# Kernel tuning notes

Measured on AMD Instinct MI355X. Metric: run time of the kernel, lower is better.

The kernel has to match this reference:

```python
import jax, jax.numpy as jnp
import numpy as np

EPS = 1e-5
K_NEIGH = 8


def _conv1(x, w, b):
    # x: [B,C,N], w: [O,C], b: [O] -> [B,O,N]  (1x1 Conv1d)
    return jnp.einsum('bcn,oc->bon', x, w) + b[None, :, None]


def _bn(x, g, b):
    # BatchNorm1d in training mode: stats over (B, N)
    m = jnp.mean(x, axis=(0, 2), keepdims=True)
    v = jnp.var(x, axis=(0, 2), keepdims=True)
    return g[None, :, None] * (x - m) * jax.lax.rsqrt(v + EPS) + b[None, :, None]


def _get_local_diffs(x, k):
    # x: [B,N,C] -> [B, 2C, N]
    xyz = x[:, :, :3]
    sq = jnp.sum(xyz * xyz, axis=-1)  # [B,N]
    d2 = sq[:, :, None] + sq[:, None, :] - 2.0 * jnp.einsum('bnc,bmc->bnm', xyz, xyz)
    dists = jnp.sqrt(jnp.maximum(d2, 0.0))  # [B,N,N]
    _, idx = jax.lax.top_k(-dists, k + 1)   # smallest distances
    idx = idx[:, :, 1:]                     # drop self -> [B,N,k]
    neigh = jax.vmap(lambda xi, ii: xi[ii])(x, idx)  # [B,N,k,C]
    diff_mean = jnp.mean(neigh, axis=2) - x          # [B,N,C]
    out = jnp.concatenate([diff_mean, x], axis=2)    # [B,N,2C]
    return jnp.transpose(out, (0, 2, 1))             # [B,2C,N]


def _forward(x, w1, b1, g1, be1, w2, b2, g2, be2, w3, b3, g3, be3,
             qw, qb, kw, kb, vw, vb, fw, fb, aw1, ab1, aw2, ab2, fcw, fcb):
    h = _get_local_diffs(x, K_NEIGH)                 # [B,18,N]
    h = jax.nn.relu(_bn(_conv1(h, w1, b1), g1, be1))  # [B,64,N]
    h = jax.nn.relu(_bn(_conv1(h, w2, b2), g2, be2))  # [B,128,N]
    h = jax.nn.relu(_bn(_conv1(h, w3, b3), g3, be3))  # [B,256,N]
    # global attention
    Q = _conv1(h, qw, qb)  # [B,H,N]
    Kt = _conv1(h, kw, kb)
    V = _conv1(h, vw, vb)
    attn = jax.nn.softmax(jnp.einsum('bhn,bhm->bnm', Q, Kt), axis=-1)  # [B,N,N]
    o = jnp.einsum('bhm,bnm->bhn', V, attn)
    h = _conv1(o, fw, fb) + h
    # attention pooling
    a = jax.nn.relu(_conv1(h, aw1, ab1))
    s = _conv1(a, aw2, ab2)                 # [B,1,N]
    w = jax.nn.softmax(s, axis=-1)
    pooled = jnp.sum(h * w, axis=-1)        # [B,256]
    return jax.nn.relu(pooled @ fcw.T + fcb)  # [B,256]


def setup_inputs() -> dict:
    key = jax.random.key(0)
    ks = jax.random.split(key, 32)
    B, N, C = 4, 4096, 9
    HID = 128

    def p(i, shape, scale=0.05):
        return (jax.random.normal(ks[i], shape, dtype=jnp.float32) * scale)

    inp = {'x': jax.random.normal(ks[0], (B, N, C), dtype=jnp.float32)}
    dims = [(2 * C, 64), (64, 128), (128, 256)]
    for li, (ci, co) in enumerate(dims, start=1):
        inp[f'w{li}'] = p(li, (co, ci))
        inp[f'b{li}'] = p(li + 3, (co,))
        inp[f'g{li}'] = jnp.ones((co,), jnp.float32)
        inp[f'be{li}'] = jnp.zeros((co,), jnp.float32)
    Cf = 256
    inp['qw'] = p(7, (HID, Cf)); inp['qb'] = p(8, (HID,))
    inp['kw'] = p(9, (HID, Cf)); inp['kb'] = p(10, (HID,))
    inp['vw'] = p(11, (HID, Cf)); inp['vb'] = p(12, (HID,))
    inp['fw'] = p(13, (Cf, HID)); inp['fb'] = p(14, (Cf,))
    inp['aw1'] = p(15, (64, Cf)); inp['ab1'] = p(16, (64,))
    inp['aw2'] = p(17, (1, 64)); inp['ab2'] = p(18, (1,))
    inp['fcw'] = p(19, (256, Cf)); inp['fcb'] = p(20, (256,))
    return inp


def reference(x, w1, b1, g1, be1, w2, b2, g2, be2, w3, b3, g3, be3,
              qw, qb, kw, kb, vw, vb, fw, fb, aw1, ab1, aw2, ab2, fcw, fcb):
    return _forward(x, w1, b1, g1, be1, w2, b2, g2, be2, w3, b3, g3, be3,
                    qw, qb, kw, kb, vw, vb, fw, fb, aw1, ab1, aw2, ab2, fcw, fcb)
```

## Files before the change

kernel.cpp:

```cpp
#include <hip/hip_runtime.h>
#include <math.h>

constexpr int B    = 4;
constexpr int NPTS = 4096;
constexpr int NTOT = B * NPTS;
constexpr int CIN  = 9;
constexpr int C0   = 18;
constexpr int KNB  = 8;
constexpr int HID  = 128;
constexpr int QR   = 64;
constexpr int KC   = 64;
constexpr int NSPL = 4;
constexpr float EPSF = 1e-5f;

using f32x4  = __attribute__((ext_vector_type(4))) float;
using bf16x8 = __attribute__((ext_vector_type(8))) short;

__device__ inline unsigned short f2bf(float f) {
    unsigned int x = __float_as_uint(f);
    unsigned int r = (x + 0x7fffu + ((x >> 16) & 1u)) >> 16;
    return (unsigned short)r;
}
__device__ inline float bf2f(unsigned short u) {
    return __uint_as_float(((unsigned int)u) << 16);
}
__device__ inline unsigned int pack2(float a, float b) {
    return (unsigned int)f2bf(a) | ((unsigned int)f2bf(b) << 16);
}

#define GLD_LDS16(g, l) __builtin_amdgcn_global_load_lds( \
    (const __attribute__((address_space(1))) void*)(g),   \
    (__attribute__((address_space(3))) void*)(l), 16, 0, 0)

__global__ __launch_bounds__(256) void prep_kernel(const float* __restrict__ x,
                                                   float4* __restrict__ xyzw,
                                                   const float* __restrict__ w2,
                                                   const float* __restrict__ w3,
                                                   const float* __restrict__ qw,
                                                   const float* __restrict__ kw,
                                                   const float* __restrict__ vw,
                                                   const float* __restrict__ fw,
                                                   const float* __restrict__ aw1,
                                                   unsigned short* __restrict__ dst) {
    const int i = blockIdx.x * 256 + threadIdx.x;
    if (i < NTOT) {
        const float* xp = x + (size_t)i * CIN;
        const float a = xp[0], b = xp[1], c = xp[2];
        xyzw[i] = make_float4(a, b, c, a * a + b * b + c * c);
    }
    const float* src;
    int off;
    if      (i <   8192) { src = w2;  off = 0; }
    else if (i <  40960) { src = w3;  off = 8192; }
    else if (i <  73728) { src = qw;  off = 40960; }
    else if (i < 106496) { src = kw;  off = 73728; }
    else if (i < 139264) { src = vw;  off = 106496; }
    else if (i < 172032) { src = fw;  off = 139264; }
    else                 { src = aw1; off = 172032; }
    dst[i] = f2bf(src[i - off]);
}

__global__ __launch_bounds__(256) void knn3_kernel(const float* __restrict__ x,
                                                   const float4* __restrict__ xyzw,
                                                   float* __restrict__ h0) {
    __shared__ __align__(16) char lds[16384];
    const int tid = threadIdx.x;
    const int w = tid >> 6, l = tid & 63;
    const int b  = blockIdx.x >> 9;
    const int p0 = (blockIdx.x & 511) << 3;
    const int c  = l & 31;
    const int p  = w * 2 + (l >> 5);
    const int n  = p0 + p;
    const float4* xb4 = xyzw + (size_t)b * NPTS;

    const float4 q4 = xb4[n];
    const float qx = q4.x, qy = q4.y, qz = q4.z, sqn = q4.w;

    float bd[KNB];
    int   bi[KNB];
#pragma unroll
    for (int i = 0; i < KNB; ++i) { bd[i] = 3.0e38f; bi[i] = 0; }

    auto stage = [&](int buf, int t) {
#pragma unroll
        for (int i = 0; i < 2; ++i) {
            const int idx = i * 256 + w * 64 + l;
            const int m   = idx ^ ((idx >> 4) & 7);
            GLD_LDS16(xb4 + (size_t)t * 512 + m, lds + buf * 8192 + i * 4096 + w * 1024);
        }
    };

    stage(0, 0);
    for (int t = 0; t < 8; ++t) {
        const int cur = t & 1;
        __syncthreads();
        if (t < 7) stage(cur ^ 1, t + 1);

        float thr = bd[KNB - 1];
        thr = fminf(thr, __shfl_xor(thr, 1));
        thr = fminf(thr, __shfl_xor(thr, 2));
        thr = fminf(thr, __shfl_xor(thr, 4));
        thr = fminf(thr, __shfl_xor(thr, 8));
        thr = fminf(thr, __shfl_xor(thr, 16));

        const char* buf = lds + cur * 8192 + c * 256;
        const int mbase = t * 512 + c * 16;
        const int cswz  = (c & 7) << 4;
#pragma unroll 4
        for (int j = 0; j < 16; ++j) {
            const float4 f4 = *(const float4*)(buf + ((j << 4) ^ cswz));
            const float tt = fmaf(qx, f4.x, fmaf(qy, f4.y, qz * f4.z));
            const float d2 = fmaf(-2.0f, tt, sqn + f4.w);
            const int m = mbase + j;
            const float gate = fminf(thr, bd[KNB - 1]);
            if (d2 < gate && m != n) {
                bd[KNB - 1] = d2; bi[KNB - 1] = m;
#pragma unroll
                for (int s = KNB - 1; s > 0; --s) {
                    if (bd[s] < bd[s - 1]) {
                        float td = bd[s]; bd[s] = bd[s - 1]; bd[s - 1] = td;
                        int   ti = bi[s]; bi[s] = bi[s - 1]; bi[s - 1] = ti;
                    }
                }
            }
        }
    }

    int res[KNB];
    const int lh = l & 31;
#pragma unroll
    for (int r = 0; r < KNB; ++r) {
        float hd = bd[0]; int hb = bi[0]; int hl = lh;
#pragma unroll
        for (int mask = 16; mask > 0; mask >>= 1) {
            const float od = __shfl_xor(hd, mask);
            const int   ob = __shfl_xor(hb, mask);
            const int   ol = __shfl_xor(hl, mask);
            if (od < hd || (od == hd && ol < hl)) { hd = od; hb = ob; hl = ol; }
        }
        res[r] = hb;
        if (lh == hl) {
#pragma unroll
            for (int s = 0; s < KNB - 1; ++s) { bd[s] = bd[s + 1]; bi[s] = bi[s + 1]; }
            bd[KNB - 1] = 3.0e38f;
        }
    }

    const int c8 = c & 7;
    int nb = res[0];
#pragma unroll
    for (int k = 1; k < KNB; ++k) nb = (c8 == k) ? res[k] : nb;
    const float* xb = x + (size_t)b * NPTS * CIN;
    float nv[CIN];
    const float* nbp = xb + (size_t)nb * CIN;
#pragma unroll
    for (int ch = 0; ch < CIN; ++ch) nv[ch] = nbp[ch];
#pragma unroll
    for (int d = 1; d < 8; d <<= 1) {
#pragma unroll
        for (int ch = 0; ch < CIN; ++ch) nv[ch] += __shfl_xor(nv[ch], d);
    }
    const int ch = min(c, 8);
    float nvc = nv[0];
#pragma unroll
    for (int k = 1; k < CIN; ++k) nvc = (ch == k) ? nv[k] : nvc;
    if (c < 9) {
        const float xv = xb[(size_t)n * CIN + ch];
        h0[((size_t)b * C0 + ch) * NPTS + n]       = nvc * 0.125f - xv;
        h0[((size_t)b * C0 + CIN + ch) * NPTS + n] = xv;
    }
}

__global__ __launch_bounds__(256) void conv1_kernel(const float* __restrict__ X,
                                                    const float* __restrict__ W,
                                                    const float* __restrict__ bias,
                                                    float* __restrict__ Y,
                                                    float* __restrict__ parts) {
    __shared__ float Ws[16 * C0];
    const int b  = blockIdx.z;
    const int o_base = blockIdx.y * 16;
    const int l  = threadIdx.x & 63;
    const int n  = blockIdx.x * 64 + l;
    const int og = threadIdx.x >> 6;
    for (int i = threadIdx.x; i < 16 * C0; i += 256)
        Ws[i] = W[(size_t)o_base * C0 + i];
    __syncthreads();
    float acc[4] = {0.f, 0.f, 0.f, 0.f};
    const float* Xp = X + (size_t)b * C0 * NPTS + n;
    for (int c = 0; c < C0; ++c) {
        const float xv = Xp[(size_t)c * NPTS];
#pragma unroll
        for (int i = 0; i < 4; ++i)
            acc[i] = fmaf(Ws[(og * 4 + i) * C0 + c], xv, acc[i]);
    }
    f32x4 v;
#pragma unroll
    for (int i = 0; i < 4; ++i) v[i] = acc[i] + bias[o_base + og * 4 + i];
    *(f32x4*)(Y + ((size_t)b * NPTS + n) * 64 + o_base + og * 4) = v;
    float s1[4], s2[4];
#pragma unroll
    for (int i = 0; i < 4; ++i) { s1[i] = v[i]; s2[i] = v[i] * v[i]; }
#pragma unroll
    for (int d = 1; d < 64; d <<= 1) {
#pragma unroll
        for (int i = 0; i < 4; ++i) {
            s1[i] += __shfl_xor(s1[i], d);
            s2[i] += __shfl_xor(s2[i], d);
        }
    }
    if (l == 0) {
        const int rg = blockIdx.z * 64 + blockIdx.x;
#pragma unroll
        for (int i = 0; i < 4; ++i) {
            const int ch = o_base + og * 4 + i;
            parts[ch * 256 + rg]            = s1[i];
            parts[64 * 256 + ch * 256 + rg] = s2[i];
        }
    }
}

__global__ __launch_bounds__(64) void finstats_kernel(const float* __restrict__ parts,
                                                      float* __restrict__ mstats, int O) {
    const int ch = blockIdx.x, l = threadIdx.x;
    const f32x4 a1 = *(const f32x4*)(parts + (size_t)ch * 256 + l * 4);
    const f32x4 a2 = *(const f32x4*)(parts + (size_t)O * 256 + (size_t)ch * 256 + l * 4);
    float s1 = (a1[0] + a1[1]) + (a1[2] + a1[3]);
    float s2 = (a2[0] + a2[1]) + (a2[2] + a2[3]);
#pragma unroll
    for (int d = 1; d < 64; d <<= 1) {
        s1 += __shfl_xor(s1, d);
        s2 += __shfl_xor(s2, d);
    }
    if (l == 0) {
        const float mean = s1 * (1.0f / NTOT);
        const float var  = s2 * (1.0f / NTOT) - mean * mean;
        mstats[ch]     = mean;
        mstats[O + ch] = rsqrtf(var + EPSF);
    }
}

__global__ __launch_bounds__(256) void bnapply_kernel(const float* __restrict__ Y,
                                                      const float* __restrict__ mstats,
                                                      const float* __restrict__ g,
                                                      const float* __restrict__ be,
                                                      unsigned short* __restrict__ Yb,
                                                      int O) {
    const size_t i4 = (size_t)blockIdx.x * 256 + threadIdx.x;
    const int cbase = (int)((i4 * 4) & (O - 1));
    const f32x4 v = *(const f32x4*)(Y + i4 * 4);
    ushort4 pk;
    unsigned short* pp = (unsigned short*)&pk;
#pragma unroll
    for (int r = 0; r < 4; ++r) {
        const int c = cbase + r;
        const float y = fmaxf(g[c] * mstats[O + c] * (v[r] - mstats[c]) + be[c], 0.f);
        pp[r] = f2bf(y);
    }
    *(ushort4*)(Yb + i4 * 4) = pk;
}

template <int C, int EPI>
__global__ __launch_bounds__(256) void gemm_kernel(const unsigned short* __restrict__ A,
                                                   const unsigned short* __restrict__ Wb,
                                                   const float* __restrict__ bias,
                                                   const unsigned short* __restrict__ resid,
                                                   void* __restrict__ Yv, int O,
                                                   float* __restrict__ parts) {
    constexpr int RB = 2 * C;
    constexpr int SLOTS = C / 8;
    __shared__ __align__(16) char ldsW[64 * RB];
    const int tid = threadIdx.x;
    const int w = tid >> 6, l = tid & 63;
    const int lg = l >> 4, lq = l & 15;
    const int n0 = blockIdx.x * 64;
    const int o0 = blockIdx.y * 64;

#pragma unroll
    for (int i = 0; i < C / 32; ++i) {
        const int idx = i * 256 + tid;
        const int m  = idx / SLOTS;
        const int sl = (idx % SLOTS) ^ (m & 7);
        GLD_LDS16(Wb + (size_t)(o0 + m) * C + sl * 8, ldsW + (i * 256 + w * 64) * 16);
    }

    const int nr = n0 + w * 16 + lq;
    const unsigned short* Ap = A + (size_t)nr * C + lg * 8;
    f32x4 acc[4];
#pragma unroll
    for (int os = 0; os < 4; ++os) acc[os] = {0.f, 0.f, 0.f, 0.f};
    __syncthreads();

#pragma unroll
    for (int ks = 0; ks < C / 32; ++ks) {
        const bf16x8 af = *(const bf16x8*)(Ap + ks * 32);
#pragma unroll
        for (int os = 0; os < 4; ++os) {
            const int row = os * 16 + lq;
            const bf16x8 wf = *(const bf16x8*)(ldsW + ((row * RB + ks * 64 + lg * 16) ^ ((lq & 7) << 4)));
            acc[os] = __builtin_amdgcn_mfma_f32_16x16x32_bf16(wf, af, acc[os], 0, 0, 0);
        }
    }

    f32x4 vv[4];
#pragma unroll
    for (int os = 0; os < 4; ++os) {
        const int ob = o0 + os * 16 + lg * 4;
        const f32x4 bv = *(const f32x4*)(bias + ob);
#pragma unroll
        for (int r = 0; r < 4; ++r) vv[os][r] = acc[os][r] + bv[r];
        if (EPI == 0) {
            *(f32x4*)((float*)Yv + (size_t)nr * O + ob) = vv[os];
        } else if (EPI == 4) {
            unsigned short* Y = (unsigned short*)Yv;
            const int bb = nr >> 12, n = nr & (NPTS - 1);
#pragma unroll
            for (int r = 0; r < 4; ++r)
                Y[((size_t)bb * HID + ob + r) * NPTS + n] = f2bf(vv[os][r]);
        } else {
            f32x4 v = vv[os];
            if (EPI == 3) {
                const ushort4 rv = *(const ushort4*)(resid + (size_t)nr * O + ob);
                v[0] += bf2f(rv.x); v[1] += bf2f(rv.y); v[2] += bf2f(rv.z); v[3] += bf2f(rv.w);
            }
            if (EPI == 2) {
#pragma unroll
                for (int r = 0; r < 4; ++r) v[r] = fmaxf(v[r], 0.f);
            }
            ushort4 pk;
            pk.x = f2bf(v[0]); pk.y = f2bf(v[1]); pk.z = f2bf(v[2]); pk.w = f2bf(v[3]);
            *(ushort4*)((unsigned short*)Yv + (size_t)nr * O + ob) = pk;
        }
    }

    if (EPI == 0) {
        float* sred = (float*)ldsW;
        float s1[4][4], s2[4][4];
#pragma unroll
        for (int os = 0; os < 4; ++os)
#pragma unroll
            for (int r = 0; r < 4; ++r) {
                float a1 = vv[os][r], a2 = vv[os][r] * vv[os][r];
#pragma unroll
                for (int d = 1; d < 16; d <<= 1) {
                    a1 += __shfl_xor(a1, d);
                    a2 += __shfl_xor(a2, d);
                }
                s1[os][r] = a1; s2[os][r] = a2;
            }
        __syncthreads();
        if (lq == 0) {
#pragma unroll
            for (int os = 0; os < 4; ++os)
#pragma unroll
                for (int r = 0; r < 4; ++r) {
                    const int ch = os * 16 + lg * 4 + r;
                    sred[(w * 64 + ch) * 2 + 0] = s1[os][r];
                    sred[(w * 64 + ch) * 2 + 1] = s2[os][r];
                }
        }
        __syncthreads();
        if (tid < 128) {
            const int ch = tid & 63, st = tid >> 6;
            const float a = sred[ch * 2 + st] + sred[(64 + ch) * 2 + st]
                          + sred[(128 + ch) * 2 + st] + sred[(192 + ch) * 2 + st];
            parts[(size_t)st * O * 256 + (size_t)(o0 + ch) * 256 + blockIdx.x] = a;
        }
    }
}

__device__ __forceinline__ void stage_tile(char* lds, int buf,
                                           const unsigned short* Kb,
                                           const unsigned short* Vb,
                                           int n0, int w, int l) {
    char* dK = lds + buf * 16384;
    char* dV = lds + 32768 + buf * 16384;
#pragma unroll
    for (int j = 0; j < 4; ++j) {
        const int y = w * 4096 + j * 1024 + l * 16;
        const int m = y >> 8;
        const int slot = ((y >> 4) & 15) ^ (m & 7);
        GLD_LDS16(Kb + (size_t)(n0 + m) * HID + slot * 8, dK + w * 4096 + j * 1024);
    }
#pragma unroll
    for (int j = 0; j < 4; ++j) {
        const int y = w * 4096 + j * 1024 + l * 16;
        const int h = y >> 7;
        const int slot = ((y >> 4) & 7) ^ (h & 7);
        GLD_LDS16(Vb + (size_t)h * NPTS + n0 + slot * 8, dV + w * 4096 + j * 1024);
    }
}

__global__ __launch_bounds__(256) void fmha2_kernel(const unsigned short* __restrict__ Qg,
                                                    const unsigned short* __restrict__ Kg,
                                                    const unsigned short* __restrict__ Vg,
                                                    float* __restrict__ A0, float* __restrict__ A1,
                                                    float* __restrict__ A2, float* __restrict__ A3,
                                                    float* __restrict__ Mb, float* __restrict__ Lb) {
    __shared__ __align__(16) char lds[73728];
    const int tid = threadIdx.x;
    const int w = tid >> 6, l = tid & 63;
    const int lg = l >> 4, lq = l & 15;
    const int b  = blockIdx.y;
    const int q0 = blockIdx.x * QR;
    const int split = blockIdx.z;
    const int n0base = split * (NPTS / NSPL);
    float* Ap = (split == 0) ? A0 : (split == 1) ? A1 : (split == 2) ? A2 : A3;
    float* Mp = Mb + split * NTOT;
    float* Lp = Lb + split * NTOT;
    char* ldsP = lds + 65536 + w * 2048;

    bf16x8 qf[4];
    {
        const unsigned short* qp = Qg + ((size_t)b * NPTS + q0 + w * 16 + lq) * HID + lg * 8;
#pragma unroll
        for (int ks = 0; ks < 4; ++ks)
            qf[ks] = *(const bf16x8*)(qp + ks * 32);
    }
    const unsigned short* Kb = Kg + (size_t)b * NPTS * HID;
    const unsigned short* Vb = Vg + (size_t)b * HID * NPTS;

    float m_r = -3.0e38f;
    float lsum = 0.f;
    f32x4 oacc[8];
#pragma unroll
    for (int hs = 0; hs < 8; ++hs) oacc[hs] = {0.f, 0.f, 0.f, 0.f};

    constexpr int NT = (NPTS / NSPL) / KC;
    stage_tile(lds, 0, Kb, Vb, n0base, w, l);

    for (int t = 0; t < NT; ++t) {
        const int cur = t & 1;
        __syncthreads();
        if (t + 1 < NT)
            stage_tile(lds, cur ^ 1, Kb, Vb, n0base + (t + 1) * KC, w, l);
        char* ldsK = lds + cur * 16384;
        char* ldsV = lds + 32768 + cur * 16384;

        f32x4 sv[4];
        __builtin_amdgcn_s_setprio(1);
#pragma unroll
        for (int ms = 0; ms < 4; ++ms) {
            const int row = ms * 16 + lq;
            f32x4 s = {0.f, 0.f, 0.f, 0.f};
#pragma unroll
            for (int ks = 0; ks < 4; ++ks) {
                bf16x8 kf = *(const bf16x8*)(ldsK + ((row * 256 + ks * 64 + lg * 16) ^ ((row & 7) << 4)));
                s = __builtin_amdgcn_mfma_f32_16x16x32_bf16(kf, qf[ks], s, 0, 0, 0);
            }
            sv[ms] = s;
        }
        __builtin_amdgcn_s_setprio(0);

        float pmax = sv[0][0];
#pragma unroll
        for (int ms = 0; ms < 4; ++ms)
#pragma unroll
            for (int r = 0; r < 4; ++r) pmax = fmaxf(pmax, sv[ms][r]);
        pmax = fmaxf(pmax, __shfl_xor(pmax, 16));
        pmax = fmaxf(pmax, __shfl_xor(pmax, 32));

        if (__any(pmax > m_r + 8.0f)) {
            const float newm = fmaxf(m_r, pmax);
            const float sc = __expf(m_r - newm);
            lsum *= sc;
            float sc_r[4];
#pragma unroll
            for (int r = 0; r < 4; ++r) sc_r[r] = __shfl(sc, lg * 4 + r);
#pragma unroll
            for (int hs = 0; hs < 8; ++hs)
#pragma unroll
                for (int r = 0; r < 4; ++r) oacc[hs][r] *= sc_r[r];
            m_r = newm;
        }

#pragma unroll
        for (int ms = 0; ms < 4; ++ms) {
            const float p0 = __expf(sv[ms][0] - m_r);
            const float p1 = __expf(sv[ms][1] - m_r);
            const float p2 = __expf(sv[ms][2] - m_r);
            const float p3 = __expf(sv[ms][3] - m_r);
            lsum += (p0 + p1) + (p2 + p3);
            const int lin = lq * 128 + ms * 32 + lg * 8;
            const int ad  = lin ^ ((lq & 7) << 4);
            *(unsigned int*)(ldsP + ad)     = pack2(p0, p1);
            *(unsigned int*)(ldsP + ad + 4) = pack2(p2, p3);
        }

        __builtin_amdgcn_s_setprio(1);
#pragma unroll
        for (int msl = 0; msl < 2; ++msl) {
            bf16x8 pf = *(const bf16x8*)(ldsP + ((lq * 128 + msl * 64 + lg * 16) ^ ((lq & 7) << 4)));
#pragma unroll
            for (int hs = 0; hs < 8; ++hs) {
                const int hrow = hs * 16 + lq;
                bf16x8 vf = *(const bf16x8*)(ldsV + ((hrow * 128 + msl * 64 + lg * 16) ^ ((hrow & 7) << 4)));
                oacc[hs] = __builtin_amdgcn_mfma_f32_16x16x32_bf16(pf, vf, oacc[hs], 0, 0, 0);
            }
        }
        __builtin_amdgcn_s_setprio(0);
    }

    lsum += __shfl_xor(lsum, 16);
    lsum += __shfl_xor(lsum, 32);
    float* Ab = Ap + ((size_t)b * NPTS + q0 + w * 16) * HID;
#pragma unroll
    for (int hs = 0; hs < 8; ++hs) {
#pragma unroll
        for (int r = 0; r < 4; ++r)
            Ab[(size_t)(lg * 4 + r) * HID + hs * 16 + lq] = oacc[hs][r];
    }
    if (lg == 0) {
        Mp[b * NPTS + q0 + w * 16 + lq] = m_r;
        Lp[b * NPTS + q0 + w * 16 + lq] = lsum;
    }
}

__global__ __launch_bounds__(256) void fmha_combine_kernel(const float* __restrict__ A0,
                                                           const float* __restrict__ A1,
                                                           const float* __restrict__ A2,
                                                           const float* __restrict__ A3,
                                                           const float* __restrict__ Mb,
                                                           const float* __restrict__ Lb,
                                                           unsigned short* __restrict__ Ob) {
    const int i = blockIdx.x * 256 + threadIdx.x;
    const int nidx = i >> 7;
    const float m0 = Mb[nidx], m1 = Mb[NTOT + nidx];
    const float m2 = Mb[2 * NTOT + nidx], m3 = Mb[3 * NTOT + nidx];
    const float M = fmaxf(fmaxf(m0, m1), fmaxf(m2, m3));
    const float e0 = __expf(m0 - M), e1 = __expf(m1 - M);
    const float e2 = __expf(m2 - M), e3 = __expf(m3 - M);
    const float den = e0 * Lb[nidx] + e1 * Lb[NTOT + nidx]
                    + e2 * Lb[2 * NTOT + nidx] + e3 * Lb[3 * NTOT + nidx];
    const float num = e0 * A0[i] + e1 * A1[i] + e2 * A2[i] + e3 * A3[i];
    Ob[i] = f2bf(num / den);
}

__global__ __launch_bounds__(256) void aw2_kernel(const unsigned short* __restrict__ a,
                                                  const float* __restrict__ aw2,
                                                  const float* __restrict__ ab2,
                                                  float* __restrict__ s) {
    __shared__ float wsm[64];
    const int tid = threadIdx.x;
    if (tid < 64) wsm[tid] = aw2[tid];
    __syncthreads();
    const int nr = blockIdx.x * 256 + tid;
    const bf16x8* ap8 = (const bf16x8*)(a + (size_t)nr * 64);
    float acc = ab2[0];
#pragma unroll
    for (int g8 = 0; g8 < 8; ++g8) {
        const bf16x8 v = ap8[g8];
#pragma unroll
        for (int e = 0; e < 8; ++e)
            acc = fmaf(bf2f((unsigned short)v[e]), wsm[g8 * 8 + e], acc);
    }
    s[nr] = acc;
}

__global__ __launch_bounds__(256) void softmax_w_kernel(float* __restrict__ s) {
    const int b = blockIdx.x;
    const int tid = threadIdx.x;
    __shared__ float red[256];
    float lm = -3.0e38f;
    for (int n = tid; n < NPTS; n += 256) lm = fmaxf(lm, s[b * NPTS + n]);
    red[tid] = lm;
    __syncthreads();
    for (int st = 128; st > 0; st >>= 1) {
        if (tid < st) red[tid] = fmaxf(red[tid], red[tid + st]);
        __syncthreads();
    }
    const float mx = red[0];
    __syncthreads();
    float ls = 0.f;
    for (int n = tid; n < NPTS; n += 256) {
        const float p = __expf(s[b * NPTS + n] - mx);
        s[b * NPTS + n] = p;
        ls += p;
    }
    red[tid] = ls;
    __syncthreads();
    for (int st = 128; st > 0; st >>= 1) {
        if (tid < st) red[tid] += red[tid + st];
        __syncthreads();
    }
    const float inv = 1.f / red[0];
    __syncthreads();
    for (int n = tid; n < NPTS; n += 256) s[b * NPTS + n] *= inv;
}

__global__ __launch_bounds__(256) void pool3_kernel(const unsigned short* __restrict__ h,
                                                    const float* __restrict__ w,
                                                    float* __restrict__ pooled) {
    const int b  = blockIdx.y;
    const int n0 = blockIdx.x * 64;
    const int cg = (threadIdx.x & 63) * 4;
    const int rs = threadIdx.x >> 6;
    float a0 = 0.f, a1 = 0.f, a2 = 0.f, a3 = 0.f;
#pragma unroll 4
    for (int i = 0; i < 16; ++i) {
        const int n = n0 + i * 4 + rs;
        const ushort4 v = *(const ushort4*)(h + ((size_t)b * NPTS + n) * 256 + cg);
        const float wv = w[b * NPTS + n];
        a0 = fmaf(bf2f(v.x), wv, a0);
        a1 = fmaf(bf2f(v.y), wv, a1);
        a2 = fmaf(bf2f(v.z), wv, a2);
        a3 = fmaf(bf2f(v.w), wv, a3);
    }
    float* pp = pooled + b * 256 + cg;
    atomicAdd(pp + 0, a0);
    atomicAdd(pp + 1, a1);
    atomicAdd(pp + 2, a2);
    atomicAdd(pp + 3, a3);
}

__global__ __launch_bounds__(256) void fc_kernel(const float* __restrict__ pooled,
                                                 const float* __restrict__ fcw,
                                                 const float* __restrict__ fcb,
                                                 float* __restrict__ out) {
    const int b = blockIdx.x, j = threadIdx.x;
    __shared__ float ps[256];
    ps[j] = pooled[b * 256 + j];
    __syncthreads();
    float acc = fcb[j];
    for (int c = 0; c < 256; ++c) acc = fmaf(ps[c], fcw[j * 256 + c], acc);
    out[b * 256 + j] = fmaxf(acc, 0.f);
}

extern "C" void kernel_launch(void* const* d_in, const int* in_sizes, int n_in,
                              void* d_out, int out_size, void* d_ws, size_t ws_size,
                              hipStream_t stream) {
    const float* x   = (const float*)d_in[0];
    const float* w1  = (const float*)d_in[1];
    const float* b1  = (const float*)d_in[2];
    const float* g1  = (const float*)d_in[3];
    const float* be1 = (const float*)d_in[4];
    const float* w2  = (const float*)d_in[5];
    const float* b2  = (const float*)d_in[6];
    const float* g2  = (const float*)d_in[7];
    const float* be2 = (const float*)d_in[8];
    const float* w3  = (const float*)d_in[9];
    const float* b3  = (const float*)d_in[10];
    const float* g3  = (const float*)d_in[11];
    const float* be3 = (const float*)d_in[12];
    const float* qw  = (const float*)d_in[13];
    const float* qb  = (const float*)d_in[14];
    const float* kw  = (const float*)d_in[15];
    const float* kb  = (const float*)d_in[16];
    const float* vw  = (const float*)d_in[17];
    const float* vb  = (const float*)d_in[18];
    const float* fw  = (const float*)d_in[19];
    const float* fb  = (const float*)d_in[20];
    const float* aw1 = (const float*)d_in[21];
    const float* ab1 = (const float*)d_in[22];
    const float* aw2 = (const float*)d_in[23];
    const float* ab2 = (const float*)d_in[24];
    const float* fcw = (const float*)d_in[25];
    const float* fcb = (const float*)d_in[26];

    float* ws = (float*)d_ws;
    float* h0     = ws;
    float* arena1 = h0 + 294912;
    float* arena2 = arena1 + 4194304;
    float* arena3 = arena2 + 2097152;
    float* arena4 = arena3 + 1048576;
    float* arena5 = arena4 + 1048576;
    float* arena6 = arena5 + 1048576;
    float* arena7 = arena6 + 2097152;
    float* Mls    = arena7 + 2097152;
    float* s      = Mls + 131072;
    float* pooled = s + 16384;
    float* mstats = pooled + 1024;
    float* wbf    = mstats + 512;
    float* xyzwp  = wbf + 94208;
    float* parts  = xyzwp + 65536;

    float* y1 = arena1;
    float* y2 = arena1;
    float* y3 = arena1;
    unsigned short* H1b = (unsigned short*)arena3;
    unsigned short* H2b = (unsigned short*)arena3;
    unsigned short* Qb  = (unsigned short*)arena3;
    unsigned short* OBF = (unsigned short*)arena3;
    unsigned short* H3b = (unsigned short*)arena2;
    unsigned short* Kb  = (unsigned short*)arena4;
    unsigned short* AB  = (unsigned short*)arena4;
    unsigned short* Vb  = (unsigned short*)arena5;
    float* Acc0 = arena6;
    unsigned short* H4b = (unsigned short*)arena6;
    float* Acc1 = arena7;
    float* Acc2 = arena1;
    float* Acc3 = arena1 + 2097152;
    float* Mb = Mls;
    float* Lb = Mls + 4 * NTOT;
    unsigned short* WB = (unsigned short*)wbf;
    unsigned short* w2b  = WB;
    unsigned short* w3b  = WB + 8192;
    unsigned short* qwb  = WB + 40960;
    unsigned short* kwb  = WB + 73728;
    unsigned short* vwb  = WB + 106496;
    unsigned short* fwb  = WB + 139264;
    unsigned short* aw1b = WB + 172032;
    float4* xyzw = (float4*)xyzwp;

    hipMemsetAsync(pooled, 0, 1024 * sizeof(float), stream);
    prep_kernel<<<dim3(736), 256, 0, stream>>>(x, xyzw, w2, w3, qw, kw, vw, fw, aw1, WB);
    knn3_kernel<<<dim3(NTOT / 8), 256, 0, stream>>>(x, xyzw, h0);

    conv1_kernel<<<dim3(NPTS / 64, 4, B), 256, 0, stream>>>(h0, w1, b1, y1, parts);
    finstats_kernel<<<64, 64, 0, stream>>>(parts, mstats, 64);
    bnapply_kernel<<<dim3(NTOT * 64 / 1024), 256, 0, stream>>>(y1, mstats, g1, be1, H1b, 64);
    gemm_kernel<64, 0><<<dim3(NTOT / 64, 2), 256, 0, stream>>>(H1b, w2b, b2, nullptr, y2, 128, parts);
    finstats_kernel<<<128, 64, 0, stream>>>(parts, mstats, 128);
    bnapply_kernel<<<dim3(NTOT * 128 / 1024), 256, 0, stream>>>(y2, mstats, g2, be2, H2b, 128);
    gemm_kernel<128, 0><<<dim3(NTOT / 64, 4), 256, 0, stream>>>(H2b, w3b, b3, nullptr, y3, 256, parts);
    finstats_kernel<<<256, 64, 0, stream>>>(parts, mstats, 256);
    bnapply_kernel<<<dim3(NTOT * 256 / 1024), 256, 0, stream>>>(y3, mstats, g3, be3, H3b, 256);

    gemm_kernel<256, 1><<<dim3(NTOT / 64, 2), 256, 0, stream>>>(H3b, qwb, qb, nullptr, Qb, 128, nullptr);
    gemm_kernel<256, 1><<<dim3(NTOT / 64, 2), 256, 0, stream>>>(H3b, kwb, kb, nullptr, Kb, 128, nullptr);
    gemm_kernel<256, 4><<<dim3(NTOT / 64, 2), 256, 0, stream>>>(H3b, vwb, vb, nullptr, Vb, 128, nullptr);

    fmha2_kernel<<<dim3(NPTS / QR, B, NSPL), 256, 0, stream>>>(Qb, Kb, Vb, Acc0, Acc1, Acc2, Acc3, Mb, Lb);
    fmha_combine_kernel<<<dim3(NTOT * HID / 256), 256, 0, stream>>>(Acc0, Acc1, Acc2, Acc3, Mb, Lb, OBF);

    gemm_kernel<128, 3><<<dim3(NTOT / 64, 4), 256, 0, stream>>>(OBF, fwb, fb, H3b, H4b, 256, nullptr);
    gemm_kernel<256, 2><<<dim3(NTOT / 64, 1), 256, 0, stream>>>(H4b, aw1b, ab1, nullptr, AB, 64, nullptr);
    aw2_kernel<<<dim3(NTOT / 256), 256, 0, stream>>>(AB, aw2, ab2, s);

    softmax_w_kernel<<<B, 256, 0, stream>>>(s);
    pool3_kernel<<<dim3(64, B), 256, 0, stream>>>(H4b, s, pooled);
    fc_kernel<<<B, 256, 0, stream>>>(pooled, fcw, fcb, (float*)d_out);

    (void)in_sizes; (void)n_in; (void)out_size; (void)ws_size;
}
```

Measured before the change: 292.9 us.

## Fuse QKV projections, fold aw2 dot into aw1 GEMM, wave-vote kNN insert

The three Q/K/V projection GEMM launches become one qkv_kernel launch with a 6-wide grid y-dimension. The aw2 reduction is folded into the aw1 GEMM epilogue (EPI 5), which drops the intermediate AB buffer and a separate kernel. In the kNN scan, the insertion gate is hoisted and only recomputed when some lane in the wave inserts, gated by __any, to cut per-candidate overhead. These changes trade a few launches and memory round trips for slightly more complex epilogues.

```diff
diff --git a/kernel.cpp b/kernel.cpp
--- a/kernel.cpp
+++ b/kernel.cpp
@@ -103,6 +103,7 @@
         thr = fminf(thr, __shfl_xor(thr, 8));
         thr = fminf(thr, __shfl_xor(thr, 16));
 
+        float gate = fminf(thr, bd[KNB - 1]);
         const char* buf = lds + cur * 8192 + c * 256;
         const int mbase = t * 512 + c * 16;
         const int cswz  = (c & 7) << 4;
@@ -112,16 +113,19 @@
             const float tt = fmaf(qx, f4.x, fmaf(qy, f4.y, qz * f4.z));
             const float d2 = fmaf(-2.0f, tt, sqn + f4.w);
             const int m = mbase + j;
-            const float gate = fminf(thr, bd[KNB - 1]);
-            if (d2 < gate && m != n) {
-                bd[KNB - 1] = d2; bi[KNB - 1] = m;
-#pragma unroll
-                for (int s = KNB - 1; s > 0; --s) {
-                    if (bd[s] < bd[s - 1]) {
-                        float td = bd[s]; bd[s] = bd[s - 1]; bd[s - 1] = td;
-                        int   ti = bi[s]; bi[s] = bi[s - 1]; bi[s - 1] = ti;
+            const bool want = (d2 < gate) && (m != n);
+            if (__any(want)) {
+                if (want) {
+                    bd[KNB - 1] = d2; bi[KNB - 1] = m;
+#pragma unroll
+                    for (int s = KNB - 1; s > 0; --s) {
+                        if (bd[s] < bd[s - 1]) {
+                            float td = bd[s]; bd[s] = bd[s - 1]; bd[s - 1] = td;
+                            int   ti = bi[s]; bi[s] = bi[s - 1]; bi[s - 1] = ti;
+                        }
                     }
                 }
+                gate = fminf(thr, bd[KNB - 1]);
             }
         }
     }
@@ -302,6 +306,7 @@
     }
 
     f32x4 vv[4];
+    float dotacc = 0.f;
 #pragma unroll
     for (int os = 0; os < 4; ++os) {
         const int ob = o0 + os * 16 + lg * 4;
@@ -316,6 +321,11 @@
 #pragma unroll
             for (int r = 0; r < 4; ++r)
                 Y[((size_t)bb * HID + ob + r) * NPTS + n] = f2bf(vv[os][r]);
+        } else if (EPI == 5) {
+            const f32x4 w2v = *(const f32x4*)((const float*)resid + ob);
+#pragma unroll
+            for (int r = 0; r < 4; ++r)
+                dotacc = fmaf(fmaxf(vv[os][r], 0.f), w2v[r], dotacc);
         } else {
             f32x4 v = vv[os];
             if (EPI == 3) {
@@ -330,6 +340,12 @@
             pk.x = f2bf(v[0]); pk.y = f2bf(v[1]); pk.z = f2bf(v[2]); pk.w = f2bf(v[3]);
             *(ushort4*)((unsigned short*)Yv + (size_t)nr * O + ob) = pk;
         }
+    }
+
+    if (EPI == 5) {
+        dotacc += __shfl_xor(dotacc, 16);
+        dotacc += __shfl_xor(dotacc, 32);
+        if (lg == 0) ((float*)Yv)[nr] = dotacc + ((const float*)parts)[0];
     }
 
     if (EPI == 0) {
@@ -364,6 +380,73 @@
             const float a = sred[ch * 2 + st] + sred[(64 + ch) * 2 + st]
                           + sred[(128 + ch) * 2 + st] + sred[(192 + ch) * 2 + st];
             parts[(size_t)st * O * 256 + (size_t)(o0 + ch) * 256 + blockIdx.x] = a;
+        }
+    }
+}
+
+__global__ __launch_bounds__(256) void qkv_kernel(const unsigned short* __restrict__ A,
+                                                  const unsigned short* __restrict__ Wall,
+                                                  const float* __restrict__ qb,
+                                                  const float* __restrict__ kb,
+                                                  const float* __restrict__ vb,
+                                                  unsigned short* __restrict__ Qo,
+                                                  unsigned short* __restrict__ Ko,
+                                                  unsigned short* __restrict__ Vo) {
+    constexpr int C = 256, RB = 512, SLOTS = 32;
+    __shared__ __align__(16) char ldsW[64 * RB];
+    const int tid = threadIdx.x;
+    const int w = tid >> 6, l = tid & 63;
+    const int lg = l >> 4, lq = l & 15;
+    const int n0 = blockIdx.x * 64;
+    const int by = blockIdx.y;
+    const int proj = by >> 1;
+    const int o0 = (by & 1) * 64;
+    const unsigned short* Wb = Wall + (size_t)proj * 32768;
+    const float* bias = (proj == 0) ? qb : (proj == 1) ? kb : vb;
+
+#pragma unroll
+    for (int i = 0; i < C / 32; ++i) {
+        const int idx = i * 256 + tid;
+        const int m  = idx / SLOTS;
+        const int sl = (idx % SLOTS) ^ (m & 7);
+        GLD_LDS16(Wb + (size_t)(o0 + m) * C + sl * 8, ldsW + (i * 256 + w * 64) * 16);
+    }
+
+    const int nr = n0 + w * 16 + lq;
+    const unsigned short* Ap = A + (size_t)nr * C + lg * 8;
+    f32x4 acc[4];
+#pragma unroll
+    for (int os = 0; os < 4; ++os) acc[os] = {0.f, 0.f, 0.f, 0.f};
+    __syncthreads();
+
+#pragma unroll
+    for (int ks = 0; ks < C / 32; ++ks) {
+        const bf16x8 af = *(const bf16x8*)(Ap + ks * 32);
+#pragma unroll
+        for (int os = 0; os < 4; ++os) {
+            const int row = os * 16 + lq;
+            const bf16x8 wf = *(const bf16x8*)(ldsW + ((row * RB + ks * 64 + lg * 16) ^ ((lq & 7) << 4)));
+            acc[os] = __builtin_amdgcn_mfma_f32_16x16x32_bf16(wf, af, acc[os], 0, 0, 0);
+        }
+    }
+
+#pragma unroll
+    for (int os = 0; os < 4; ++os) {
+        const int ob = o0 + os * 16 + lg * 4;
+        const f32x4 bv = *(const f32x4*)(bias + ob);
+        f32x4 v;
+#pragma unroll
+        for (int r = 0; r < 4; ++r) v[r] = acc[os][r] + bv[r];
+        if (proj < 2) {
+            unsigned short* Y = proj ? Ko : Qo;
+            ushort4 pk;
+            pk.x = f2bf(v[0]); pk.y = f2bf(v[1]); pk.z = f2bf(v[2]); pk.w = f2bf(v[3]);
+            *(ushort4*)(Y + (size_t)nr * 128 + ob) = pk;
+        } else {
+            const int bb = nr >> 12, n = nr & (NPTS - 1);
+#pragma unroll
+            for (int r = 0; r < 4; ++r)
+                Vo[((size_t)bb * HID + ob + r) * NPTS + n] = f2bf(v[r]);
         }
     }
 }
@@ -533,27 +616,6 @@
                     + e2 * Lb[2 * NTOT + nidx] + e3 * Lb[3 * NTOT + nidx];
     const float num = e0 * A0[i] + e1 * A1[i] + e2 * A2[i] + e3 * A3[i];
     Ob[i] = f2bf(num / den);
-}
-
-__global__ __launch_bounds__(256) void aw2_kernel(const unsigned short* __restrict__ a,
-                                                  const float* __restrict__ aw2,
-                                                  const float* __restrict__ ab2,
-                                                  float* __restrict__ s) {
-    __shared__ float wsm[64];
-    const int tid = threadIdx.x;
-    if (tid < 64) wsm[tid] = aw2[tid];
-    __syncthreads();
-    const int nr = blockIdx.x * 256 + tid;
-    const bf16x8* ap8 = (const bf16x8*)(a + (size_t)nr * 64);
-    float acc = ab2[0];
-#pragma unroll
-    for (int g8 = 0; g8 < 8; ++g8) {
-        const bf16x8 v = ap8[g8];
-#pragma unroll
-        for (int e = 0; e < 8; ++e)
-            acc = fmaf(bf2f((unsigned short)v[e]), wsm[g8 * 8 + e], acc);
-    }
-    s[nr] = acc;
 }
 
 __global__ __launch_bounds__(256) void softmax_w_kernel(float* __restrict__ s) {
@@ -682,7 +744,6 @@
     unsigned short* OBF = (unsigned short*)arena3;
     unsigned short* H3b = (unsigned short*)arena2;
     unsigned short* Kb  = (unsigned short*)arena4;
-    unsigned short* AB  = (unsigned short*)arena4;
     unsigned short* Vb  = (unsigned short*)arena5;
     float* Acc0 = arena6;
     unsigned short* H4b = (unsigned short*)arena6;
@@ -695,8 +756,6 @@
     unsigned short* w2b  = WB;
     unsigned short* w3b  = WB + 8192;
     unsigned short* qwb  = WB + 40960;
-    unsigned short* kwb  = WB + 73728;
-    unsigned short* vwb  = WB + 106496;
     unsigned short* fwb  = WB + 139264;
     unsigned short* aw1b = WB + 172032;
     float4* xyzw = (float4*)xyzwp;
@@ -715,16 +774,14 @@
     finstats_kernel<<<256, 64, 0, stream>>>(parts, mstats, 256);
     bnapply_kernel<<<dim3(NTOT * 256 / 1024), 256, 0, stream>>>(y3, mstats, g3, be3, H3b, 256);
 
-    gemm_kernel<256, 1><<<dim3(NTOT / 64, 2), 256, 0, stream>>>(H3b, qwb, qb, nullptr, Qb, 128, nullptr);
-    gemm_kernel<256, 1><<<dim3(NTOT / 64, 2), 256, 0, stream>>>(H3b, kwb, kb, nullptr, Kb, 128, nullptr);
-    gemm_kernel<256, 4><<<dim3(NTOT / 64, 2), 256, 0, stream>>>(H3b, vwb, vb, nullptr, Vb, 128, nullptr);
+    qkv_kernel<<<dim3(NTOT / 64, 6), 256, 0, stream>>>(H3b, qwb, qb, kb, vb, Qb, Kb, Vb);
 
     fmha2_kernel<<<dim3(NPTS / QR, B, NSPL), 256, 0, stream>>>(Qb, Kb, Vb, Acc0, Acc1, Acc2, Acc3, Mb, Lb);
     fmha_combine_kernel<<<dim3(NTOT * HID / 256), 256, 0, stream>>>(Acc0, Acc1, Acc2, Acc3, Mb, Lb, OBF);
 
     gemm_kernel<128, 3><<<dim3(NTOT / 64, 4), 256, 0, stream>>>(OBF, fwb, fb, H3b, H4b, 256, nullptr);
-    gemm_kernel<256, 2><<<dim3(NTOT / 64, 1), 256, 0, stream>>>(H4b, aw1b, ab1, nullptr, AB, 64, nullptr);
-    aw2_kernel<<<dim3(NTOT / 256), 256, 0, stream>>>(AB, aw2, ab2, s);
+    gemm_kernel<256, 5><<<dim3(NTOT / 64, 1), 256, 0, stream>>>(H4b, aw1b, ab1,
+                                                                (const unsigned short*)aw2, s, 64, (float*)ab2);
 
     softmax_w_kernel<<<B, 256, 0, stream>>>(s);
     pool3_kernel<<<dim3(64, B), 256, 0, stream>>>(H4b, s, pooled);
```

After: 287.6 us. No clear change (-1.8%).
